# Kernel optimization log

Measured on AMD Instinct MI355X. Metric: run time of the kernel, lower is better.

## Reference

```python
import jax, jax.numpy as jnp
import numpy as np

S, P, T, E, H = 32, 48, 8, 64, 64      # scenes, peds/scene, obs_len, embedding_dim, h_dim
D1, D2 = 512, 1024                      # mlp_pre_pool hidden / bottleneck dims
B = S * P
TOTAL_LEN = 20                          # obs_len + pred_len (8 + 12)


def setup_inputs() -> dict:
    key = jax.random.key(0)
    ks = jax.random.split(key, 10)
    h_states = jax.random.normal(ks[0], (1, B, H), jnp.float32)
    end_pos = jax.random.normal(ks[1], (B, 2), jnp.float32)
    traj = jax.random.normal(ks[2], (TOTAL_LEN, B, 2), jnp.float32)
    traj_weight = jax.random.uniform(ks[3], (S, P * P, 2, T), jnp.float32)
    starts = jnp.arange(S, dtype=jnp.int32) * P
    seq_start_end = jnp.stack([starts, starts + P], axis=1)  # uniform scenes of P peds
    # learned params
    W_se = jax.random.normal(ks[4], (T * E, 2 * T), jnp.float32) * 0.05  # spatial_embedding
    b_se = jnp.zeros((T * E,), jnp.float32)
    W1 = jax.random.normal(ks[5], (D1, T * E + H), jnp.float32) * 0.05   # 576 -> 512
    b1 = jnp.zeros((D1,), jnp.float32)
    W2 = jax.random.normal(ks[6], (D2, D1), jnp.float32) * 0.05          # 512 -> 1024
    b2 = jnp.zeros((D2,), jnp.float32)
    return {"h_states": h_states, "seq_start_end": seq_start_end, "end_pos": end_pos,
            "traj": traj, "traj_weight": traj_weight, "mlp_pre_pool_dim_0": T * E,
            "W_se": W_se, "b_se": b_se, "W1": W1, "b1": b1, "W2": W2, "b2": b2}


def reference(h_states, seq_start_end, end_pos, traj, traj_weight, mlp_pre_pool_dim_0,
              W_se, b_se, W1, b1, W2, b2):
    # obs_traj: (obs_len, B, 2) -> (B, T, 2) -> per-scene (S, P, T, 2)
    obs = traj[:T].transpose(1, 0, 2).reshape(S, P, T, 2)
    h = h_states.reshape(S, P, H)
    # pairwise history differences: row (i, j) = obs[j] - obs[i]  (gather-diff)
    rel = obs[:, None, :, :, :] - obs[:, :, None, :, :]          # (S, i, j, T, 2)
    rel = rel.reshape(S, P, P, 2 * T)                            # flatten (T,2) -> 2T
    emb = rel @ W_se.T + b_se                                    # (S, P, P, T*E)
    # traj_weight[i]: (P*P, 2, T) -> permute(0,2,1) -> tile channel to E -> flatten
    w = jnp.transpose(traj_weight, (0, 1, 3, 2))                 # (S, P*P, T, 2)
    w = jnp.tile(w, (1, 1, 1, E // 2)).reshape(S, P, P, T * E)
    emb = w * emb
    # curr_hidden_1: hidden of ped j broadcast over i
    hj = jnp.broadcast_to(h[:, None, :, :], (S, P, P, H))
    x = jnp.concatenate([emb, hj], axis=-1)                      # (S, P, P, 576)
    x = jax.nn.relu(x @ W1.T + b1)                               # (S, P, P, 512)
    x = jax.nn.relu(x @ W2.T + b2)                               # (S, P, P, 1024)
    pool_h = x.max(axis=2)                                       # max over j
    return pool_h.reshape(S * P, D2)
```

## Files before the change

kernel.cpp:

```cpp
#include <hip/hip_runtime.h>
#include <hip/hip_bf16.h>
#include <stdint.h>

#define S_  32
#define P_  48
#define T_  8
#define E_  64
#define H_  64
#define D1_ 512
#define D2_ 1024
#define B_  (S_*P_)
#define M_  (S_*P_*P_)
#define K1_ 576
#define KE_ 512

typedef __attribute__((ext_vector_type(8))) short  short8;
typedef __attribute__((ext_vector_type(4))) short  short4v;
typedef __attribute__((ext_vector_type(8))) __bf16 bf16x8;
typedef __attribute__((ext_vector_type(4))) float  f32x4;
typedef __attribute__((ext_vector_type(8))) float  f32x8;

__device__ inline short f2bf(float x) {
  union { float f; unsigned u; } v; v.f = x;
  unsigned r = v.u + 0x7FFFu + ((v.u >> 16) & 1u);
  return (short)(r >> 16);
}

__device__ inline void async16(const void* g, void* l) {
  __builtin_amdgcn_global_load_lds(
      (const __attribute__((address_space(1))) void*)g,
      (__attribute__((address_space(3))) void*)l, 16, 0, 0);
}

__device__ inline f32x4 mfma16(short8 a, short8 b, f32x4 c) {
  return __builtin_amdgcn_mfma_f32_16x16x32_bf16(
      __builtin_bit_cast(bf16x8, a), __builtin_bit_cast(bf16x8, b), c, 0, 0, 0);
}

__global__ __launch_bounds__(256) void k_cvt_w(const float* __restrict__ W1,
                                               const float* __restrict__ W2,
                                               short* __restrict__ W1b,
                                               short* __restrict__ W2b) {
  int idx = blockIdx.x * 256 + threadIdx.x;
  if (idx < D1_ * K1_) W1b[idx] = f2bf(W1[idx]);
  int idx2 = idx - D1_ * K1_;
  if (idx2 >= 0 && idx2 < D2_ * D1_) W2b[idx2] = f2bf(W2[idx2]);
}

__global__ __launch_bounds__(256) void k_oW(const float* __restrict__ traj,
                                            const float* __restrict__ Wse,
                                            float* __restrict__ oW) {
  int bid = blockIdx.x;
  int p = bid >> 1;
  int n = ((bid & 1) << 8) + threadIdx.x;
  float obs[16];
#pragma unroll
  for (int t = 0; t < T_; ++t) {
    obs[2*t]   = traj[(t*B_ + p)*2 + 0];
    obs[2*t+1] = traj[(t*B_ + p)*2 + 1];
  }
  float acc = 0.f;
#pragma unroll
  for (int k = 0; k < 16; ++k) acc += obs[k] * Wse[n*16 + k];
  oW[p*KE_ + n] = acc;
}

__global__ __launch_bounds__(256) void k_build_x(const float* __restrict__ tw,
                                                 const float* __restrict__ h,
                                                 const float* __restrict__ bse,
                                                 const float* __restrict__ oW,
                                                 short* __restrict__ X) {
  int tid = threadIdx.x;
  int wid = tid >> 6, lane = tid & 63;
  int row = blockIdx.x * 4 + wid;
  int s   = row / (P_ * P_);
  int rem = row - s * (P_ * P_);
  int i   = rem / P_;
  int j   = rem - i * P_;
  int bi = s * P_ + i, bj = s * P_ + j;

  const float* twq = tw + (size_t)(s * (P_*P_) + rem) * 16;
  int t = lane >> 3;
  float w0 = twq[t];
  float w1 = twq[8 + t];

  int n0 = lane * 8;
  f32x8 vj = *(const f32x8*)&oW[(size_t)bj * KE_ + n0];
  f32x8 vi = *(const f32x8*)&oW[(size_t)bi * KE_ + n0];
  f32x8 vb = *(const f32x8*)&bse[n0];
  short8 o;
#pragma unroll
  for (int k = 0; k < 8; ++k) {
    float e = (vj[k] - vi[k] + vb[k]) * ((k & 1) ? w1 : w0);
    o[k] = f2bf(e);
  }
  *(short8*)&X[(size_t)row * K1_ + n0] = o;

  if (lane < 8) {
    f32x8 vh = *(const f32x8*)&h[(size_t)bj * H_ + lane * 8];
    short8 oh;
#pragma unroll
    for (int k = 0; k < 8; ++k) oh[k] = f2bf(vh[k]);
    *(short8*)&X[(size_t)row * K1_ + KE_ + lane * 8] = oh;
  }
}

__global__ __launch_bounds__(512, 2) void k_gemm1(const short* __restrict__ X,
                                                  const short* __restrict__ W1b,
                                                  const float* __restrict__ b1,
                                                  short* __restrict__ X1) {
  __shared__ short Abuf[2][288 * 64];
  __shared__ short Bbuf[2][256 * 64];
  int tid = threadIdx.x;
  int wid = tid >> 6, lane = tid & 63;
  int wgid = (blockIdx.x & 7) * 64 + (blockIdx.x >> 3);
  int tm = wgid >> 1, tn = wgid & 1;
  int brow = tm * 288, bcol = tn * 256;
  int wrm = wid >> 2, wcn = wid & 3;
  int lr = lane & 15, lhi = lane >> 4;
  int sx = lr & 7;

  f32x4 acc[9][4];
#pragma unroll
  for (int m = 0; m < 9; ++m)
#pragma unroll
    for (int n = 0; n < 4; ++n) acc[m][n] = (f32x4){0.f, 0.f, 0.f, 0.f};

  auto stageA = [&](int buf, int k0) {
#pragma unroll
    for (int it = 0; it < 4; ++it) {
      int fg = it * 512 + tid;
      int r = fg >> 3, gs = (fg & 7) ^ (r & 7);
      async16(&X[(size_t)(brow + r) * K1_ + k0 + (gs << 3)], &Abuf[buf][fg * 8]);
    }
    if (tid < 256) {
      int fg = 2048 + tid;
      int r = fg >> 3, gs = (fg & 7) ^ (r & 7);
      async16(&X[(size_t)(brow + r) * K1_ + k0 + (gs << 3)], &Abuf[buf][fg * 8]);
    }
  };
  auto stageB = [&](int buf, int k0) {
#pragma unroll
    for (int it = 0; it < 4; ++it) {
      int fg = it * 512 + tid;
      int r = fg >> 3, gs = (fg & 7) ^ (r & 7);
      async16(&W1b[(size_t)(bcol + r) * K1_ + k0 + (gs << 3)], &Bbuf[buf][fg * 8]);
    }
  };
  auto compute = [&](int buf) {
#pragma unroll
    for (int kk = 0; kk < 2; ++kk) {
      int gr = kk * 4 + lhi;
      short8 a[9], b[4];
#pragma unroll
      for (int m = 0; m < 9; ++m)
        a[m] = *(const short8*)&Abuf[buf][(wrm*144 + m*16 + lr) * 64 + ((gr ^ sx) << 3)];
#pragma unroll
      for (int n = 0; n < 4; ++n)
        b[n] = *(const short8*)&Bbuf[buf][(wcn*64 + n*16 + lr) * 64 + ((gr ^ sx) << 3)];
      __builtin_amdgcn_s_setprio(1);
#pragma unroll
      for (int m = 0; m < 9; ++m)
#pragma unroll
        for (int n = 0; n < 4; ++n)
          acc[m][n] = mfma16(b[n], a[m], acc[m][n]);
      __builtin_amdgcn_s_setprio(0);
    }
  };

  const int NT = 9;
  stageA(0, 0); stageB(0, 0);
  asm volatile("s_waitcnt vmcnt(0)" ::: "memory");
  __builtin_amdgcn_s_barrier();
  for (int t = 0; t < NT; ++t) {
    int bf = t & 1;
    if (t + 1 < NT) { stageA(bf ^ 1, (t + 1) * 64); stageB(bf ^ 1, (t + 1) * 64); }
    compute(bf);
    asm volatile("s_waitcnt vmcnt(0)" ::: "memory");
    __builtin_amdgcn_s_barrier();
  }

#pragma unroll
  for (int m = 0; m < 9; ++m) {
    int grow = brow + wrm*144 + m*16 + lr;
#pragma unroll
    for (int n = 0; n < 4; ++n) {
      int colbase = bcol + wcn*64 + n*16 + lhi*4;
      f32x4 bias = *(const f32x4*)&b1[colbase];
      short4v o;
#pragma unroll
      for (int q = 0; q < 4; ++q) {
        float v = acc[m][n][q] + bias[q];
        v = v > 0.f ? v : 0.f;
        o[q] = f2bf(v);
      }
      *(short4v*)&X1[(size_t)grow * D1_ + colbase] = o;
    }
  }
}

__global__ __launch_bounds__(512, 2) void k_gemm2(const short* __restrict__ X1,
                                                  const short* __restrict__ W2b,
                                                  const float* __restrict__ b2,
                                                  float* __restrict__ out) {
  __shared__ short Abuf[2][288 * 64];
  __shared__ short Bbuf[2][256 * 64];
  int tid = threadIdx.x;
  int wid = tid >> 6, lane = tid & 63;
  int wgid = (blockIdx.x & 7) * 128 + (blockIdx.x >> 3);
  int tm = wgid >> 2, tn = wgid & 3;
  int brow = tm * 288, bcol = tn * 256;
  int wrm = wid >> 2, wcn = wid & 3;
  int lr = lane & 15, lhi = lane >> 4;
  int sx = lr & 7;

  f32x4 acc[9][4];
#pragma unroll
  for (int m = 0; m < 9; ++m)
#pragma unroll
    for (int n = 0; n < 4; ++n) acc[m][n] = (f32x4){0.f, 0.f, 0.f, 0.f};

  auto stageA = [&](int buf, int k0) {
#pragma unroll
    for (int it = 0; it < 4; ++it) {
      int fg = it * 512 + tid;
      int r = fg >> 3, gs = (fg & 7) ^ (r & 7);
      async16(&X1[(size_t)(brow + r) * D1_ + k0 + (gs << 3)], &Abuf[buf][fg * 8]);
    }
    if (tid < 256) {
      int fg = 2048 + tid;
      int r = fg >> 3, gs = (fg & 7) ^ (r & 7);
      async16(&X1[(size_t)(brow + r) * D1_ + k0 + (gs << 3)], &Abuf[buf][fg * 8]);
    }
  };
  auto stageB = [&](int buf, int k0) {
#pragma unroll
    for (int it = 0; it < 4; ++it) {
      int fg = it * 512 + tid;
      int r = fg >> 3, gs = (fg & 7) ^ (r & 7);
      async16(&W2b[(size_t)(bcol + r) * D1_ + k0 + (gs << 3)], &Bbuf[buf][fg * 8]);
    }
  };
  auto compute = [&](int buf) {
#pragma unroll
    for (int kk = 0; kk < 2; ++kk) {
      int gr = kk * 4 + lhi;
      short8 a[9], b[4];
#pragma unroll
      for (int m = 0; m < 9; ++m)
        a[m] = *(const short8*)&Abuf[buf][(wrm*144 + m*16 + lr) * 64 + ((gr ^ sx) << 3)];
#pragma unroll
      for (int n = 0; n < 4; ++n)
        b[n] = *(const short8*)&Bbuf[buf][(wcn*64 + n*16 + lr) * 64 + ((gr ^ sx) << 3)];
      __builtin_amdgcn_s_setprio(1);
#pragma unroll
      for (int m = 0; m < 9; ++m)
#pragma unroll
        for (int n = 0; n < 4; ++n)
          acc[m][n] = mfma16(a[m], b[n], acc[m][n]);
      __builtin_amdgcn_s_setprio(0);
    }
  };

  const int NT = 8;
  stageA(0, 0); stageB(0, 0);
  asm volatile("s_waitcnt vmcnt(0)" ::: "memory");
  __builtin_amdgcn_s_barrier();
  for (int t = 0; t < NT; ++t) {
    int bf = t & 1;
    if (t + 1 < NT) { stageA(bf ^ 1, (t + 1) * 64); stageB(bf ^ 1, (t + 1) * 64); }
    compute(bf);
    asm volatile("s_waitcnt vmcnt(0)" ::: "memory");
    __builtin_amdgcn_s_barrier();
  }

  int gbase = tm * 6 + wrm * 3;
#pragma unroll
  for (int n = 0; n < 4; ++n) {
    int gcol = bcol + wcn*64 + n*16 + lr;
    float bias = b2[gcol];
    float gm[3] = {0.f, 0.f, 0.f};
#pragma unroll
    for (int m = 0; m < 9; ++m) {
      float r = 0.f;
#pragma unroll
      for (int q = 0; q < 4; ++q) {
        float v = acc[m][n][q] + bias;
        if (v > r) r = v;
      }
      int g = m / 3;
      if (r > gm[g]) gm[g] = r;
    }
#pragma unroll
    for (int g = 0; g < 3; ++g) {
      float r = gm[g];
      r = fmaxf(r, __shfl_xor(r, 16));
      r = fmaxf(r, __shfl_xor(r, 32));
      if (lhi == 0) out[(size_t)(gbase + g) * D2_ + gcol] = r;
    }
  }
}

extern "C" void kernel_launch(void* const* d_in, const int* in_sizes, int n_in,
                              void* d_out, int out_size, void* d_ws, size_t ws_size,
                              hipStream_t stream) {
  const float* h_states = (const float*)d_in[0];
  const float* traj = (const float*)d_in[3];
  const float* tw   = (const float*)d_in[4];
  const float* Wse  = (const float*)d_in[6];
  const float* bse  = (const float*)d_in[7];
  const float* W1   = (const float*)d_in[8];
  const float* b1   = (const float*)d_in[9];
  const float* W2   = (const float*)d_in[10];
  const float* b2   = (const float*)d_in[11];
  float* out = (float*)d_out;

  char* ws = (char*)d_ws;
  const size_t X_BYTES   = (size_t)M_ * K1_ * 2;
  const size_t X1_BYTES  = (size_t)M_ * D1_ * 2;
  const size_t W1B_BYTES = (size_t)D1_ * K1_ * 2;
  short* X   = (short*)ws;
  short* X1  = (short*)(ws + X_BYTES);
  short* W1b = (short*)(ws + X_BYTES + X1_BYTES);
  short* W2b = (short*)(ws + X_BYTES + X1_BYTES + W1B_BYTES);
  float* oW  = (float*)(ws + X_BYTES);

  k_cvt_w  <<<(D1_*K1_ + D2_*D1_ + 255) / 256, 256, 0, stream>>>(W1, W2, W1b, W2b);
  k_oW     <<<B_ * 2, 256, 0, stream>>>(traj, Wse, oW);
  k_build_x<<<M_ / 4, 256, 0, stream>>>(tw, h_states, bse, oW, X);
  k_gemm1  <<<(M_ / 288) * (D1_ / 256), 512, 0, stream>>>(X, W1b, b1, X1);
  k_gemm2  <<<(M_ / 288) * (D2_ / 256), 512, 0, stream>>>(X1, W2b, b2, out);
}
```

Measured before the change: 260.4 us.

## Switch GEMMs to 32x32x16 MFMA with 192-row tiles

Both GEMM kernels move from 16x16x32 bf16 MFMA to 32x32x16 bf16 MFMA, and the M tile shrinks from 288 to 192 rows, giving each wave a 96x64 sub-tile and fewer, larger accumulators. The LDS fragment loads, the epilogue layout and the max-pool reduction are rewritten to match the 32x32 output layout. The goal is fewer LDS reads per FLOP, less MFMA issue overhead and more workgroups for load balance. In exchange, each tile reuses less data and makes more global loads, and the fused max-over-j epilogue now has to track the 48-row group boundary inside the middle 32-row block.

```diff
diff --git a/kernel.cpp b/kernel.cpp
--- a/kernel.cpp
+++ b/kernel.cpp
@@ -14,11 +14,12 @@
 #define K1_ 576
 #define KE_ 512
 
-typedef __attribute__((ext_vector_type(8))) short  short8;
-typedef __attribute__((ext_vector_type(4))) short  short4v;
-typedef __attribute__((ext_vector_type(8))) __bf16 bf16x8;
-typedef __attribute__((ext_vector_type(4))) float  f32x4;
-typedef __attribute__((ext_vector_type(8))) float  f32x8;
+typedef __attribute__((ext_vector_type(8)))  short  short8;
+typedef __attribute__((ext_vector_type(4)))  short  short4v;
+typedef __attribute__((ext_vector_type(8)))  __bf16 bf16x8;
+typedef __attribute__((ext_vector_type(4)))  float  f32x4;
+typedef __attribute__((ext_vector_type(8)))  float  f32x8;
+typedef __attribute__((ext_vector_type(16))) float  f32x16;
 
 __device__ inline short f2bf(float x) {
   union { float f; unsigned u; } v; v.f = x;
@@ -32,8 +33,8 @@
       (__attribute__((address_space(3))) void*)l, 16, 0, 0);
 }
 
-__device__ inline f32x4 mfma16(short8 a, short8 b, f32x4 c) {
-  return __builtin_amdgcn_mfma_f32_16x16x32_bf16(
+__device__ inline f32x16 mfma32(short8 a, short8 b, f32x16 c) {
+  return __builtin_amdgcn_mfma_f32_32x32x16_bf16(
       __builtin_bit_cast(bf16x8, a), __builtin_bit_cast(bf16x8, b), c, 0, 0, 0);
 }
 
@@ -109,32 +110,29 @@
                                                   const short* __restrict__ W1b,
                                                   const float* __restrict__ b1,
                                                   short* __restrict__ X1) {
-  __shared__ short Abuf[2][288 * 64];
+  __shared__ short Abuf[2][192 * 64];
   __shared__ short Bbuf[2][256 * 64];
   int tid = threadIdx.x;
   int wid = tid >> 6, lane = tid & 63;
-  int wgid = (blockIdx.x & 7) * 64 + (blockIdx.x >> 3);
+  int wgid = (blockIdx.x & 7) * 96 + (blockIdx.x >> 3);
   int tm = wgid >> 1, tn = wgid & 1;
-  int brow = tm * 288, bcol = tn * 256;
+  int brow = tm * 192, bcol = tn * 256;
   int wrm = wid >> 2, wcn = wid & 3;
-  int lr = lane & 15, lhi = lane >> 4;
-  int sx = lr & 7;
-
-  f32x4 acc[9][4];
-#pragma unroll
-  for (int m = 0; m < 9; ++m)
-#pragma unroll
-    for (int n = 0; n < 4; ++n) acc[m][n] = (f32x4){0.f, 0.f, 0.f, 0.f};
+  int c31 = lane & 31, hi = lane >> 5;
+  int sx = lane & 7;
+
+  f32x16 acc[3][2];
+#pragma unroll
+  for (int m = 0; m < 3; ++m)
+#pragma unroll
+    for (int n = 0; n < 2; ++n)
+#pragma unroll
+      for (int e = 0; e < 16; ++e) acc[m][n][e] = 0.f;
 
   auto stageA = [&](int buf, int k0) {
 #pragma unroll
-    for (int it = 0; it < 4; ++it) {
+    for (int it = 0; it < 3; ++it) {
       int fg = it * 512 + tid;
-      int r = fg >> 3, gs = (fg & 7) ^ (r & 7);
-      async16(&X[(size_t)(brow + r) * K1_ + k0 + (gs << 3)], &Abuf[buf][fg * 8]);
-    }
-    if (tid < 256) {
-      int fg = 2048 + tid;
       int r = fg >> 3, gs = (fg & 7) ^ (r & 7);
       async16(&X[(size_t)(brow + r) * K1_ + k0 + (gs << 3)], &Abuf[buf][fg * 8]);
     }
@@ -149,21 +147,25 @@
   };
   auto compute = [&](int buf) {
 #pragma unroll
-    for (int kk = 0; kk < 2; ++kk) {
-      int gr = kk * 4 + lhi;
-      short8 a[9], b[4];
-#pragma unroll
-      for (int m = 0; m < 9; ++m)
-        a[m] = *(const short8*)&Abuf[buf][(wrm*144 + m*16 + lr) * 64 + ((gr ^ sx) << 3)];
-#pragma unroll
-      for (int n = 0; n < 4; ++n)
-        b[n] = *(const short8*)&Bbuf[buf][(wcn*64 + n*16 + lr) * 64 + ((gr ^ sx) << 3)];
+    for (int ks = 0; ks < 4; ++ks) {
+      int g = (2 * ks + hi) ^ sx;
+      short8 a[3], b[2];
+#pragma unroll
+      for (int m = 0; m < 3; ++m) {
+        int row = wrm * 96 + m * 32 + c31;
+        a[m] = *(const short8*)&Abuf[buf][row * 64 + (g << 3)];
+      }
+#pragma unroll
+      for (int n = 0; n < 2; ++n) {
+        int rowb = wcn * 64 + n * 32 + c31;
+        b[n] = *(const short8*)&Bbuf[buf][rowb * 64 + (g << 3)];
+      }
       __builtin_amdgcn_s_setprio(1);
 #pragma unroll
-      for (int m = 0; m < 9; ++m)
-#pragma unroll
-        for (int n = 0; n < 4; ++n)
-          acc[m][n] = mfma16(b[n], a[m], acc[m][n]);
+      for (int m = 0; m < 3; ++m)
+#pragma unroll
+        for (int n = 0; n < 2; ++n)
+          acc[m][n] = mfma32(b[n], a[m], acc[m][n]);
       __builtin_amdgcn_s_setprio(0);
     }
   };
@@ -181,21 +183,23 @@
   }
 
 #pragma unroll
-  for (int m = 0; m < 9; ++m) {
-    int grow = brow + wrm*144 + m*16 + lr;
-#pragma unroll
-    for (int n = 0; n < 4; ++n) {
-      int colbase = bcol + wcn*64 + n*16 + lhi*4;
-      f32x4 bias = *(const f32x4*)&b1[colbase];
-      short4v o;
-#pragma unroll
-      for (int q = 0; q < 4; ++q) {
-        float v = acc[m][n][q] + bias[q];
-        v = v > 0.f ? v : 0.f;
-        o[q] = f2bf(v);
-      }
-      *(short4v*)&X1[(size_t)grow * D1_ + colbase] = o;
-    }
+  for (int m = 0; m < 3; ++m) {
+    int grow = brow + wrm * 96 + m * 32 + c31;
+#pragma unroll
+    for (int n = 0; n < 2; ++n)
+#pragma unroll
+      for (int rq = 0; rq < 4; ++rq) {
+        int colb = bcol + wcn * 64 + n * 32 + 8 * rq + 4 * hi;
+        f32x4 bias = *(const f32x4*)&b1[colb];
+        short4v o;
+#pragma unroll
+        for (int e = 0; e < 4; ++e) {
+          float v = acc[m][n][rq * 4 + e] + bias[e];
+          v = v > 0.f ? v : 0.f;
+          o[e] = f2bf(v);
+        }
+        *(short4v*)&X1[(size_t)grow * D1_ + colb] = o;
+      }
   }
 }
 
@@ -203,32 +207,29 @@
                                                   const short* __restrict__ W2b,
                                                   const float* __restrict__ b2,
                                                   float* __restrict__ out) {
-  __shared__ short Abuf[2][288 * 64];
+  __shared__ short Abuf[2][192 * 64];
   __shared__ short Bbuf[2][256 * 64];
   int tid = threadIdx.x;
   int wid = tid >> 6, lane = tid & 63;
-  int wgid = (blockIdx.x & 7) * 128 + (blockIdx.x >> 3);
+  int wgid = (blockIdx.x & 7) * 192 + (blockIdx.x >> 3);
   int tm = wgid >> 2, tn = wgid & 3;
-  int brow = tm * 288, bcol = tn * 256;
+  int brow = tm * 192, bcol = tn * 256;
   int wrm = wid >> 2, wcn = wid & 3;
-  int lr = lane & 15, lhi = lane >> 4;
-  int sx = lr & 7;
-
-  f32x4 acc[9][4];
-#pragma unroll
-  for (int m = 0; m < 9; ++m)
-#pragma unroll
-    for (int n = 0; n < 4; ++n) acc[m][n] = (f32x4){0.f, 0.f, 0.f, 0.f};
+  int c31 = lane & 31, hi = lane >> 5;
+  int sx = lane & 7;
+
+  f32x16 acc[3][2];
+#pragma unroll
+  for (int m = 0; m < 3; ++m)
+#pragma unroll
+    for (int n = 0; n < 2; ++n)
+#pragma unroll
+      for (int e = 0; e < 16; ++e) acc[m][n][e] = 0.f;
 
   auto stageA = [&](int buf, int k0) {
 #pragma unroll
-    for (int it = 0; it < 4; ++it) {
+    for (int it = 0; it < 3; ++it) {
       int fg = it * 512 + tid;
-      int r = fg >> 3, gs = (fg & 7) ^ (r & 7);
-      async16(&X1[(size_t)(brow + r) * D1_ + k0 + (gs << 3)], &Abuf[buf][fg * 8]);
-    }
-    if (tid < 256) {
-      int fg = 2048 + tid;
       int r = fg >> 3, gs = (fg & 7) ^ (r & 7);
       async16(&X1[(size_t)(brow + r) * D1_ + k0 + (gs << 3)], &Abuf[buf][fg * 8]);
     }
@@ -243,21 +244,25 @@
   };
   auto compute = [&](int buf) {
 #pragma unroll
-    for (int kk = 0; kk < 2; ++kk) {
-      int gr = kk * 4 + lhi;
-      short8 a[9], b[4];
-#pragma unroll
-      for (int m = 0; m < 9; ++m)
-        a[m] = *(const short8*)&Abuf[buf][(wrm*144 + m*16 + lr) * 64 + ((gr ^ sx) << 3)];
-#pragma unroll
-      for (int n = 0; n < 4; ++n)
-        b[n] = *(const short8*)&Bbuf[buf][(wcn*64 + n*16 + lr) * 64 + ((gr ^ sx) << 3)];
+    for (int ks = 0; ks < 4; ++ks) {
+      int g = (2 * ks + hi) ^ sx;
+      short8 a[3], b[2];
+#pragma unroll
+      for (int m = 0; m < 3; ++m) {
+        int row = wrm * 96 + m * 32 + c31;
+        a[m] = *(const short8*)&Abuf[buf][row * 64 + (g << 3)];
+      }
+#pragma unroll
+      for (int n = 0; n < 2; ++n) {
+        int rowb = wcn * 64 + n * 32 + c31;
+        b[n] = *(const short8*)&Bbuf[buf][rowb * 64 + (g << 3)];
+      }
       __builtin_amdgcn_s_setprio(1);
 #pragma unroll
-      for (int m = 0; m < 9; ++m)
-#pragma unroll
-        for (int n = 0; n < 4; ++n)
-          acc[m][n] = mfma16(a[m], b[n], acc[m][n]);
+      for (int m = 0; m < 3; ++m)
+#pragma unroll
+        for (int n = 0; n < 2; ++n)
+          acc[m][n] = mfma32(a[m], b[n], acc[m][n]);
       __builtin_amdgcn_s_setprio(0);
     }
   };
@@ -274,29 +279,27 @@
     __builtin_amdgcn_s_barrier();
   }
 
-  int gbase = tm * 6 + wrm * 3;
-#pragma unroll
-  for (int n = 0; n < 4; ++n) {
-    int gcol = bcol + wcn*64 + n*16 + lr;
+  int gb = tm * 4 + wrm * 2;
+#pragma unroll
+  for (int n = 0; n < 2; ++n) {
+    int gcol = bcol + wcn * 64 + n * 32 + c31;
     float bias = b2[gcol];
-    float gm[3] = {0.f, 0.f, 0.f};
-#pragma unroll
-    for (int m = 0; m < 9; ++m) {
-      float r = 0.f;
-#pragma unroll
-      for (int q = 0; q < 4; ++q) {
-        float v = acc[m][n][q] + bias;
-        if (v > r) r = v;
-      }
-      int g = m / 3;
-      if (r > gm[g]) gm[g] = r;
-    }
-#pragma unroll
-    for (int g = 0; g < 3; ++g) {
-      float r = gm[g];
-      r = fmaxf(r, __shfl_xor(r, 16));
-      r = fmaxf(r, __shfl_xor(r, 32));
-      if (lhi == 0) out[(size_t)(gbase + g) * D2_ + gcol] = r;
+    float r0 = 0.f, r1 = 0.f;
+#pragma unroll
+    for (int e = 0; e < 16; ++e) {
+      float v0 = acc[0][n][e] + bias;
+      float v1 = acc[2][n][e] + bias;
+      float vm = acc[1][n][e] + bias;
+      if (v0 > r0) r0 = v0;
+      if (v1 > r1) r1 = v1;
+      if (e < 8) { if (vm > r0) r0 = vm; }
+      else       { if (vm > r1) r1 = vm; }
+    }
+    r0 = fmaxf(r0, __shfl_xor(r0, 32));
+    r1 = fmaxf(r1, __shfl_xor(r1, 32));
+    if (hi == 0) {
+      out[(size_t)(gb    ) * D2_ + gcol] = r0;
+      out[(size_t)(gb + 1) * D2_ + gcol] = r1;
     }
   }
 }
@@ -328,6 +331,6 @@
   k_cvt_w  <<<(D1_*K1_ + D2_*D1_ + 255) / 256, 256, 0, stream>>>(W1, W2, W1b, W2b);
   k_oW     <<<B_ * 2, 256, 0, stream>>>(traj, Wse, oW);
   k_build_x<<<M_ / 4, 256, 0, stream>>>(tw, h_states, bse, oW, X);
-  k_gemm1  <<<(M_ / 288) * (D1_ / 256), 512, 0, stream>>>(X, W1b, b1, X1);
-  k_gemm2  <<<(M_ / 288) * (D2_ / 256), 512, 0, stream>>>(X1, W2b, b2, out);
-}
+  k_gemm1  <<<(M_ / 192) * (D1_ / 256), 512, 0, stream>>>(X, W1b, b1, X1);
+  k_gemm2  <<<(M_ / 192) * (D2_ / 256), 512, 0, stream>>>(X1, W2b, b2, out);
+}
```

Measured after the change: 262.7 us. No clear change (+0.9%).
